# Optimization experiments

Hardware: AMD Instinct MI355X
Metric: run time of the kernel (lower is better)

The kernel has to match this reference:

```python
import jax, jax.numpy as jnp
import numpy as np

D = 512      # d_model
H = 8        # num_heads
HD = D // H  # head_dim = 64 (concat makes per-head dim 2*HD=128)
B = 32       # batch*group
T = 512      # time steps


def setup_inputs() -> dict:
    key = jax.random.key(0)
    ks = jax.random.split(key, 18)
    def W(k):
        return jax.random.normal(k, (D, D), dtype=jnp.float32) * 0.02
    inp = {
        "x_face": jax.random.normal(ks[0], (B, T, D), dtype=jnp.float32),
        "x_skeleton": jax.random.normal(ks[1], (B, T, D), dtype=jnp.float32),
        "wq1": W(ks[2]), "bq1": jnp.zeros((D,), jnp.float32),
        "wk1": W(ks[3]), "bk1": jnp.zeros((D,), jnp.float32),
        "wv1": W(ks[4]), "bv1": jnp.zeros((D,), jnp.float32),
        "wq2": W(ks[5]), "bq2": jnp.zeros((D,), jnp.float32),
        "wk2": W(ks[6]), "bk2": jnp.zeros((D,), jnp.float32),
        "wv2": W(ks[7]), "bv2": jnp.zeros((D,), jnp.float32),
        "wo1": W(ks[8]), "bo1": jnp.zeros((D,), jnp.float32),
        "wo2": W(ks[9]), "bo2": jnp.zeros((D,), jnp.float32),
    }
    return inp


def reference(x_face, x_skeleton,
              wq1, bq1, wk1, bk1, wv1, bv1,
              wq2, bq2, wk2, bk2, wv2, bv2,
              wo1, bo1, wo2, bo2):
    Bt, Tt, _ = x_face.shape

    def proj(x, w, b):
        # torch Linear: x @ W^T + b, then 'b t (h d) -> b h t d'
        return (x @ w.T + b).reshape(Bt, Tt, H, HD).transpose(0, 2, 1, 3)

    q = jnp.concatenate([proj(x_face, wq1, bq1), proj(x_skeleton, wq2, bq2)], axis=3)  # [B,H,T,2*HD]
    k = jnp.concatenate([proj(x_face, wk1, bk1), proj(x_skeleton, wk2, bk2)], axis=3)
    v = jnp.concatenate([proj(x_face, wv1, bv1), proj(x_skeleton, wv2, bv2)], axis=3)

    scores = jnp.einsum('bhid,bhjd->bhij', q, k) / (HD ** 0.5)  # scale by head_dim**0.5 as in source
    attn = jax.nn.softmax(scores, axis=-1)                      # dropout = identity (eval mode)
    out = jnp.einsum('bhij,bhjd->bhid', attn, v)                # [B,H,T,2*HD]
    out = out.transpose(0, 2, 1, 3).reshape(Bt, Tt, 2 * D)      # 'b h t d -> b t (h d)'

    x1, x2 = out[..., :D], out[..., D:]
    return (x1 @ wo1.T + bo1, x2 @ wo2.T + bo2)
```

## Files before the change

kernel.cpp:

```cpp
#include <hip/hip_runtime.h>
#include <hip/hip_bf16.h>
#include <stdint.h>

typedef __hip_bfloat16 bf16;
using f32x4 = __attribute__((ext_vector_type(4))) float;
using s16x8 = __attribute__((ext_vector_type(8))) short;

typedef __attribute__((address_space(1))) unsigned int gu32;
typedef __attribute__((address_space(3))) unsigned int lu32;

__device__ __forceinline__ void gll16(const void* g, void* l) {
  __builtin_amdgcn_global_load_lds((const gu32*)g, (lu32*)l, 16, 0, 0);
}

struct ConvJob { const float* src; bf16* dst; int n4; int pad; };
struct ConvParams { ConvJob j[10]; };
struct alignas(8) Bf4 { bf16 v[4]; };

__global__ void convert_kernel(ConvParams p) {
  ConvJob jb = p.j[blockIdx.z];
  int stride = gridDim.x * blockDim.x;
  for (int i = blockIdx.x * blockDim.x + threadIdx.x; i < jb.n4; i += stride) {
    float4 v = ((const float4*)jb.src)[i];
    Bf4 o;
    o.v[0] = __float2bfloat16(v.x);
    o.v[1] = __float2bfloat16(v.y);
    o.v[2] = __float2bfloat16(v.z);
    o.v[3] = __float2bfloat16(v.w);
    ((Bf4*)jb.dst)[i] = o;
  }
}

struct GemmSlice {
  const bf16* A; const bf16* W; const float* bias;
  bf16* dstQ; float* dstF;
  long lda; int dhalf; float scale; int mode;
};
struct GemmParams { GemmSlice s[6]; };

#define GSTAGE(kb) do { \
    _Pragma("unroll") \
    for (int i_ = 0; i_ < 4; ++i_) { \
      const int r0_ = w * 32 + i_ * 8; \
      gll16(Abase + (long)r0_ * lda + (kb) * 64, sA + r0_ * 64); \
      gll16(Wbase + (long)r0_ * 512 + (kb) * 64, sB + r0_ * 64); \
    } \
  } while (0)

#define GCOMPUTE() do { \
  _Pragma("unroll") \
  for (int ks = 0; ks < 2; ++ks) { \
    s16x8 af[4], bg[4]; \
    _Pragma("unroll") \
    for (int mi = 0; mi < 4; ++mi) { \
      const int row_ = wm + mi * 16 + fr; \
      af[mi] = *(const s16x8*)(sA + row_ * 64 + ((ks * 32 + fq * 8) ^ ((row_ & 7) << 3))); \
    } \
    _Pragma("unroll") \
    for (int ni = 0; ni < 4; ++ni) { \
      const int row_ = wn + ni * 16 + fr; \
      bg[ni] = *(const s16x8*)(sB + row_ * 64 + ((ks * 32 + fq * 8) ^ ((row_ & 7) << 3))); \
    } \
    __builtin_amdgcn_s_setprio(1); \
    _Pragma("unroll") \
    for (int mi = 0; mi < 4; ++mi) \
      _Pragma("unroll") \
      for (int ni = 0; ni < 4; ++ni) \
        acc[mi][ni] = __builtin_amdgcn_mfma_f32_16x16x32_bf16(af[mi], bg[ni], acc[mi][ni], 0, 0, 0); \
    __builtin_amdgcn_s_setprio(0); \
  } \
} while (0)

__global__ __launch_bounds__(256, 4) void gemm_kernel(GemmParams p) {
  __shared__ alignas(16) bf16 lds[16384];
  bf16* const sA = lds;
  bf16* const sB = lds + 8192;
  const GemmSlice sl = p.s[blockIdx.z];
  const long lda = sl.lda;
  const int tid = threadIdx.x;
  const int w = tid >> 6, ln = tid & 63;
  const int gm0 = blockIdx.x * 128;
  const int gn0 = blockIdx.y * 128;
  const int arow = ln >> 3;
  const int acolS = ((ln & 7) ^ (ln >> 3)) * 8;
  const int wm = (w >> 1) * 64, wn = (w & 1) * 64;
  const int fr = ln & 15, fq = ln >> 4;
  const bf16* const Abase = sl.A + (long)(gm0 + arow) * lda + acolS;
  const bf16* const Wbase = sl.W + (long)(gn0 + arow) * 512 + acolS;
  f32x4 acc[4][4] = {};

  for (int kb = 0; kb < 8; ++kb) {
    GSTAGE(kb);
    __syncthreads();
    GCOMPUTE();
    __syncthreads();
  }

  bf16* const eW = lds + w * 2304;
  if (sl.mode == 0) {
    const int col0 = gn0 + wn;
    const int h = col0 >> 6;
    const int bh = ((gm0 >> 9) << 3) + h;
    const int tb = (gm0 & 511) + wm;
#pragma unroll
    for (int ps = 0; ps < 2; ++ps) {
#pragma unroll
      for (int mi2 = 0; mi2 < 2; ++mi2) {
        const int mi = ps * 2 + mi2;
#pragma unroll
        for (int ni = 0; ni < 4; ++ni) {
          const float bia = sl.bias[col0 + ni * 16 + fr];
#pragma unroll
          for (int r = 0; r < 4; ++r)
            eW[(mi2 * 16 + fq * 4 + r) * 72 + ni * 16 + fr] =
                __float2bfloat16((acc[mi][ni][r] + bia) * sl.scale);
        }
      }
#pragma unroll
      for (int pp = 0; pp < 4; ++pp) {
        const int rr = pp * 8 + (ln >> 3);
        const s16x8 v = *(const s16x8*)(eW + rr * 72 + (ln & 7) * 8);
        *(s16x8*)(sl.dstQ + (((long)bh * 512 + tb + ps * 32 + rr) << 7) + sl.dhalf + (ln & 7) * 8) = v;
      }
    }
  } else if (sl.mode == 2) {
    const int col0 = gn0 + wn;
    const int h = col0 >> 6;
    const int bh = ((gm0 >> 9) << 3) + h;
    const int tb = (gm0 & 511) + wm;
#pragma unroll
    for (int ps = 0; ps < 2; ++ps) {
#pragma unroll
      for (int ni2 = 0; ni2 < 2; ++ni2) {
        const int ni = ps * 2 + ni2;
        const float bia = sl.bias[col0 + ni * 16 + fr];
#pragma unroll
        for (int mi = 0; mi < 4; ++mi) {
          Bf4 o;
#pragma unroll
          for (int r = 0; r < 4; ++r) o.v[r] = __float2bfloat16(acc[mi][ni][r] + bia);
          *(Bf4*)(eW + (ni2 * 16 + fr) * 72 + mi * 16 + fq * 4) = o;
        }
      }
#pragma unroll
      for (int pp = 0; pp < 4; ++pp) {
        const int rr = pp * 8 + (ln >> 3);
        const s16x8 v = *(const s16x8*)(eW + rr * 72 + (ln & 7) * 8);
        *(s16x8*)(sl.dstQ + (((long)bh * 128 + sl.dhalf + ps * 32 + rr) << 9) + tb + (ln & 7) * 8) = v;
      }
    }
  } else {
#pragma unroll
    for (int mi = 0; mi < 4; ++mi)
#pragma unroll
      for (int ni = 0; ni < 4; ++ni) {
        const int col = gn0 + wn + ni * 16 + fr;
        const float bia = sl.bias[col];
#pragma unroll
        for (int r = 0; r < 4; ++r) {
          const int row = gm0 + wm + mi * 16 + fq * 4 + r;
          sl.dstF[(long)row * 512 + col] = acc[mi][ni][r] + bia;
        }
      }
  }
}

#define STAGE(kt, bK, bV) do { \
    _Pragma("unroll") \
    for (int p_ = 0; p_ < 4; ++p_) \
      gll16(kgb + (kt) * 8192 + p_ * 2048, (bK) + tid * 8 + p_ * 2048); \
    _Pragma("unroll") \
    for (int p_ = 0; p_ < 4; ++p_) \
      gll16(vgb + (kt) * 64 + p_ * 16384, (bV) + tid * 8 + p_ * 2048); \
  } while (0)

#define COMPUTE(bK, bV) do { \
  f32x4 s2[2][4] = {}; \
  _Pragma("unroll") \
  for (int ks = 0; ks < 4; ++ks) { \
    _Pragma("unroll") \
    for (int ni = 0; ni < 4; ++ni) { \
      const int row_ = ni * 16 + fr; \
      const s16x8 kf = *(const s16x8*)((bK) + row_ * 128 + ((ks * 32 + fq * 8) ^ ((row_ & 7) << 3))); \
      _Pragma("unroll") \
      for (int mi = 0; mi < 2; ++mi) \
        s2[mi][ni] = __builtin_amdgcn_mfma_f32_16x16x32_bf16(qf[mi][ks], kf, s2[mi][ni], 0, 0, 0); \
    } \
  } \
  _Pragma("unroll") \
  for (int mi = 0; mi < 2; ++mi) \
    _Pragma("unroll") \
    for (int ni = 0; ni < 4; ++ni) \
      _Pragma("unroll") \
      for (int r = 0; r < 4; ++r) { \
        const int rp = mi * 16 + fq * 4 + r; \
        sPw[rp * 64 + ((ni * 16 + fr) ^ ((rp & 7) << 3))] = \
            __float2bfloat16(__builtin_amdgcn_exp2f(s2[mi][ni][r])); \
      } \
  _Pragma("unroll") \
  for (int ks = 0; ks < 2; ++ks) { \
    s16x8 pf[2]; \
    _Pragma("unroll") \
    for (int mi = 0; mi < 2; ++mi) { \
      const int row_ = mi * 16 + fr; \
      pf[mi] = *(const s16x8*)(sPw + row_ * 64 + ((ks * 32 + fq * 8) ^ ((row_ & 7) << 3))); \
      lracc[mi] = __builtin_amdgcn_mfma_f32_16x16x32_bf16(pf[mi], onesf, lracc[mi], 0, 0, 0); \
    } \
    _Pragma("unroll") \
    for (int nj = 0; nj < 8; ++nj) { \
      const int row_ = nj * 16 + fr; \
      const s16x8 vf = *(const s16x8*)((bV) + row_ * 64 + ((ks * 32 + fq * 8) ^ ((row_ & 7) << 3))); \
      _Pragma("unroll") \
      for (int mi = 0; mi < 2; ++mi) \
        o[mi][nj] = __builtin_amdgcn_mfma_f32_16x16x32_bf16(pf[mi], vf, o[mi][nj], 0, 0, 0); \
    } \
  } \
} while (0)

__global__ __launch_bounds__(256, 2) void attn_kernel(const bf16* __restrict__ Q,
                                                      const bf16* __restrict__ K,
                                                      const bf16* __restrict__ Vt,
                                                      bf16* __restrict__ AO) {
  __shared__ alignas(16) bf16 lds[40960];
  bf16* const ldsK0 = lds;
  bf16* const ldsV0 = lds + 8192;
  bf16* const ldsK1 = lds + 16384;
  bf16* const ldsV1 = lds + 24576;
  bf16* const sP    = lds + 32768;
  const int tid = threadIdx.x;
  const int w = tid >> 6, ln = tid & 63;
  const int fr = ln & 15, fq = ln >> 4;
  const int lg = (blockIdx.x & 7) * 128 + (blockIdx.x >> 3);
  const int bh = lg >> 2;
  const int q0 = (lg & 3) * 128;
  const long base = (long)bh << 16;
  bf16* const sPw = sP + w * 2048;

  const int kr0 = tid >> 4, kc = tid & 15;
  const int vr0 = tid >> 3, vc = tid & 7;
  const bf16* const kgb = K + base + kr0 * 128 + ((kc ^ (kr0 & 7)) * 8);
  const bf16* const vgb = Vt + base + (long)vr0 * 512 + ((vc ^ (vr0 & 7)) * 8);

  {
    const bf16* const qgb = Q + base + (long)q0 * 128 + kr0 * 128 + ((kc ^ (kr0 & 7)) * 8);
#pragma unroll
    for (int p = 0; p < 8; ++p)
      gll16(qgb + p * 2048, lds + tid * 8 + p * 2048);
  }
  __syncthreads();
  s16x8 qf[2][4];
#pragma unroll
  for (int mi = 0; mi < 2; ++mi) {
    const int row = w * 32 + mi * 16 + fr;
#pragma unroll
    for (int ks = 0; ks < 4; ++ks)
      qf[mi][ks] = *(const s16x8*)(lds + row * 128 + ((ks * 32 + fq * 8) ^ ((row & 7) << 3)));
  }
  __syncthreads();

  f32x4 o[2][8] = {};
  f32x4 lracc[2] = {};
  const short one_bf16 = (short)0x3F80;
  const s16x8 onesf = { one_bf16, one_bf16, one_bf16, one_bf16,
                        one_bf16, one_bf16, one_bf16, one_bf16 };

  STAGE(0, ldsK0, ldsV0);
  STAGE(1, ldsK1, ldsV1);

  for (int kt = 0; kt < 7; ++kt) {
    const bf16* bK = (kt & 1) ? ldsK1 : ldsK0;
    const bf16* bV = (kt & 1) ? ldsV1 : ldsV0;
    asm volatile("s_waitcnt vmcnt(8)" ::: "memory");
    __builtin_amdgcn_sched_barrier(0);
    __builtin_amdgcn_s_barrier();
    COMPUTE(bK, bV);
    asm volatile("s_waitcnt lgkmcnt(0)" ::: "memory");
    __builtin_amdgcn_sched_barrier(0);
    __builtin_amdgcn_s_barrier();
    if (kt < 6) STAGE(kt + 2, (bf16*)bK, (bf16*)bV);
  }
  asm volatile("s_waitcnt vmcnt(0)" ::: "memory");
  __builtin_amdgcn_sched_barrier(0);
  __builtin_amdgcn_s_barrier();
  COMPUTE(ldsK1, ldsV1);

  const int b = bh >> 3, h = bh & 7;
  float rl[2][4];
#pragma unroll
  for (int mi = 0; mi < 2; ++mi)
#pragma unroll
    for (int r = 0; r < 4; ++r) rl[mi][r] = 1.f / lracc[mi][r];
#pragma unroll
  for (int hh = 0; hh < 2; ++hh) {
#pragma unroll
    for (int mi = 0; mi < 2; ++mi)
#pragma unroll
      for (int nj4 = 0; nj4 < 4; ++nj4)
#pragma unroll
        for (int r = 0; r < 4; ++r) {
          const int rp = mi * 16 + fq * 4 + r;
          sPw[rp * 64 + ((nj4 * 16 + fr) ^ ((rp & 7) << 3))] =
              __float2bfloat16(o[mi][hh * 4 + nj4][r] * rl[mi][r]);
        }
#pragma unroll
    for (int pp = 0; pp < 4; ++pp) {
      const int rr = pp * 8 + (ln >> 3);
      const s16x8 v = *(const s16x8*)(sPw + rr * 64 + (((ln & 7) * 8) ^ ((rr & 7) << 3)));
      *(s16x8*)(AO + (((long)(b * 512 + q0 + w * 32 + rr)) << 10) + h * 128 + hh * 64 + (ln & 7) * 8) = v;
    }
  }
}

extern "C" void kernel_launch(void* const* d_in, const int* in_sizes, int n_in,
                              void* d_out, int out_size, void* d_ws, size_t ws_size,
                              hipStream_t stream) {
  const float* xf = (const float*)d_in[0];
  const float* xs = (const float*)d_in[1];
  const float* w_f[8] = { (const float*)d_in[2], (const float*)d_in[4], (const float*)d_in[6],
                          (const float*)d_in[8], (const float*)d_in[10], (const float*)d_in[12],
                          (const float*)d_in[14], (const float*)d_in[16] };

  bf16* ws = (bf16*)d_ws;
  bf16* XF = ws;
  bf16* XS = ws + 8388608;
  bf16* WW = ws + 16777216;
  bf16* Qb = ws + 18874368;
  bf16* Kb = Qb + 16777216;
  bf16* Vb = Kb + 16777216;
  bf16* AO = ws;

  ConvParams cp;
  cp.j[0] = { xf, XF, 2097152, 0 };
  cp.j[1] = { xs, XS, 2097152, 0 };
  for (int i = 0; i < 8; ++i) cp.j[2 + i] = { w_f[i], WW + i * 262144, 65536, 0 };
  convert_kernel<<<dim3(512, 1, 10), 256, 0, stream>>>(cp);

  const float qsc = 0.125f * 1.44269504088896f;
  GemmParams gp;
  gp.s[0] = { XF, WW + 0 * 262144, (const float*)d_in[3],  Qb, nullptr, 512, 0,  qsc, 0 };
  gp.s[1] = { XS, WW + 3 * 262144, (const float*)d_in[9],  Qb, nullptr, 512, 64, qsc, 0 };
  gp.s[2] = { XF, WW + 1 * 262144, (const float*)d_in[5],  Kb, nullptr, 512, 0,  1.f, 0 };
  gp.s[3] = { XS, WW + 4 * 262144, (const float*)d_in[11], Kb, nullptr, 512, 64, 1.f, 0 };
  gp.s[4] = { XF, WW + 2 * 262144, (const float*)d_in[7],  Vb, nullptr, 512, 0,  1.f, 2 };
  gp.s[5] = { XS, WW + 5 * 262144, (const float*)d_in[13], Vb, nullptr, 512, 64, 1.f, 2 };
  gemm_kernel<<<dim3(128, 4, 6), 256, 0, stream>>>(gp);

  attn_kernel<<<dim3(1024), 256, 0, stream>>>(Qb, Kb, Vb, AO);

  float* out = (float*)d_out;
  GemmParams op;
  op.s[0] = { AO,       WW + 6 * 262144, (const float*)d_in[15], nullptr, out,           1024, 0, 1.f, 1 };
  op.s[1] = { AO + 512, WW + 7 * 262144, (const float*)d_in[17], nullptr, out + 8388608, 1024, 0, 1.f, 1 };
  op.s[2] = op.s[0]; op.s[3] = op.s[0]; op.s[4] = op.s[0]; op.s[5] = op.s[0];
  gemm_kernel<<<dim3(128, 4, 2), 256, 0, stream>>>(op);
}
```

Before: 154.1 us.

## Replace LDS double buffer with register-staged prefetch in attention kernel

The attention kernel's K/V pipeline moves from two LDS buffers filled by direct global-to-LDS loads to one LDS buffer plus a register prefetch. The next tile is loaded into registers during compute and written to LDS after a barrier. This cuts LDS use per block from 80KB to 48KB, aiming at higher occupancy, but adds VGPR pressure, explicit LDS writes and an extra barrier per iteration. The wait counts must still cover the register loads correctly.

```diff
diff --git a/kernel.cpp b/kernel.cpp
--- a/kernel.cpp
+++ b/kernel.cpp
@@ -165,23 +165,37 @@
   }
 }
 
-#define STAGE(kt, bK, bV) do { \
+#define STAGE(kt) do { \
     _Pragma("unroll") \
     for (int p_ = 0; p_ < 4; ++p_) \
-      gll16(kgb + (kt) * 8192 + p_ * 2048, (bK) + tid * 8 + p_ * 2048); \
+      gll16(kgb + (kt) * 8192 + p_ * 2048, ldsK + tid * 8 + p_ * 2048); \
     _Pragma("unroll") \
     for (int p_ = 0; p_ < 4; ++p_) \
-      gll16(vgb + (kt) * 64 + p_ * 16384, (bV) + tid * 8 + p_ * 2048); \
+      gll16(vgb + (kt) * 64 + p_ * 16384, ldsV + tid * 8 + p_ * 2048); \
   } while (0)
 
-#define COMPUTE(bK, bV) do { \
+#define LOADR(kt) do { \
+    _Pragma("unroll") \
+    for (int p_ = 0; p_ < 4; ++p_) kreg[p_] = *(const s16x8*)(kgb + (kt) * 8192 + p_ * 2048); \
+    _Pragma("unroll") \
+    for (int p_ = 0; p_ < 4; ++p_) vreg[p_] = *(const s16x8*)(vgb + (kt) * 64 + p_ * 16384); \
+  } while (0)
+
+#define WRITER() do { \
+    _Pragma("unroll") \
+    for (int p_ = 0; p_ < 4; ++p_) *(s16x8*)(ldsK + tid * 8 + p_ * 2048) = kreg[p_]; \
+    _Pragma("unroll") \
+    for (int p_ = 0; p_ < 4; ++p_) *(s16x8*)(ldsV + tid * 8 + p_ * 2048) = vreg[p_]; \
+  } while (0)
+
+#define COMPUTE() do { \
   f32x4 s2[2][4] = {}; \
   _Pragma("unroll") \
   for (int ks = 0; ks < 4; ++ks) { \
     _Pragma("unroll") \
     for (int ni = 0; ni < 4; ++ni) { \
       const int row_ = ni * 16 + fr; \
-      const s16x8 kf = *(const s16x8*)((bK) + row_ * 128 + ((ks * 32 + fq * 8) ^ ((row_ & 7) << 3))); \
+      const s16x8 kf = *(const s16x8*)(ldsK + row_ * 128 + ((ks * 32 + fq * 8) ^ ((row_ & 7) << 3))); \
       _Pragma("unroll") \
       for (int mi = 0; mi < 2; ++mi) \
         s2[mi][ni] = __builtin_amdgcn_mfma_f32_16x16x32_bf16(qf[mi][ks], kf, s2[mi][ni], 0, 0, 0); \
@@ -209,7 +223,7 @@
     _Pragma("unroll") \
     for (int nj = 0; nj < 8; ++nj) { \
       const int row_ = nj * 16 + fr; \
-      const s16x8 vf = *(const s16x8*)((bV) + row_ * 64 + ((ks * 32 + fq * 8) ^ ((row_ & 7) << 3))); \
+      const s16x8 vf = *(const s16x8*)(ldsV + row_ * 64 + ((ks * 32 + fq * 8) ^ ((row_ & 7) << 3))); \
       _Pragma("unroll") \
       for (int mi = 0; mi < 2; ++mi) \
         o[mi][nj] = __builtin_amdgcn_mfma_f32_16x16x32_bf16(pf[mi], vf, o[mi][nj], 0, 0, 0); \
@@ -221,12 +235,10 @@
                                                       const bf16* __restrict__ K,
                                                       const bf16* __restrict__ Vt,
                                                       bf16* __restrict__ AO) {
-  __shared__ alignas(16) bf16 lds[40960];
-  bf16* const ldsK0 = lds;
-  bf16* const ldsV0 = lds + 8192;
-  bf16* const ldsK1 = lds + 16384;
-  bf16* const ldsV1 = lds + 24576;
-  bf16* const sP    = lds + 32768;
+  __shared__ alignas(16) bf16 lds[24576];
+  bf16* const ldsK = lds;
+  bf16* const ldsV = lds + 8192;
+  bf16* const sP   = lds + 16384;
   const int tid = threadIdx.x;
   const int w = tid >> 6, ln = tid & 63;
   const int fr = ln & 15, fq = ln >> 4;
@@ -263,26 +275,29 @@
   const short one_bf16 = (short)0x3F80;
   const s16x8 onesf = { one_bf16, one_bf16, one_bf16, one_bf16,
                         one_bf16, one_bf16, one_bf16, one_bf16 };
-
-  STAGE(0, ldsK0, ldsV0);
-  STAGE(1, ldsK1, ldsV1);
-
-  for (int kt = 0; kt < 7; ++kt) {
-    const bf16* bK = (kt & 1) ? ldsK1 : ldsK0;
-    const bf16* bV = (kt & 1) ? ldsV1 : ldsV0;
-    asm volatile("s_waitcnt vmcnt(8)" ::: "memory");
-    __builtin_amdgcn_sched_barrier(0);
-    __builtin_amdgcn_s_barrier();
-    COMPUTE(bK, bV);
+  s16x8 kreg[4], vreg[4];
+
+  STAGE(0);
+  __builtin_amdgcn_sched_barrier(0);
+  LOADR(1);
+  __builtin_amdgcn_sched_barrier(0);
+  asm volatile("s_waitcnt vmcnt(8)" ::: "memory");
+  __builtin_amdgcn_sched_barrier(0);
+  __builtin_amdgcn_s_barrier();
+
+  for (int kt = 0; kt < 8; ++kt) {
+    COMPUTE();
     asm volatile("s_waitcnt lgkmcnt(0)" ::: "memory");
     __builtin_amdgcn_sched_barrier(0);
     __builtin_amdgcn_s_barrier();
-    if (kt < 6) STAGE(kt + 2, (bf16*)bK, (bf16*)bV);
-  }
-  asm volatile("s_waitcnt vmcnt(0)" ::: "memory");
-  __builtin_amdgcn_sched_barrier(0);
-  __builtin_amdgcn_s_barrier();
-  COMPUTE(ldsK1, ldsV1);
+    if (kt < 7) {
+      WRITER();
+      if (kt < 6) LOADR(kt + 2);
+      asm volatile("s_waitcnt lgkmcnt(0)" ::: "memory");
+      __builtin_amdgcn_sched_barrier(0);
+      __builtin_amdgcn_s_barrier();
+    }
+  }
 
   const int b = bh >> 3, h = bh & 7;
   float rl[2][4];
```

Result: no change. 156.5 us (+1.6%).

## Double-buffer GEMM k-loop with async LDS loads and narrower K tiles

Applied to the files above, without the earlier changes.

Restructures the projection GEMM main loop from a single-buffered 64-wide K tile with two barriers per step into a double-buffered pipeline of 32-wide K tiles. Global-to-LDS loads for tile k+2 are issued while tile k is computed, gated by explicit vmcnt waits and barriers. The LDS swizzle is redone for the 32-column layout. This aims to hide global load latency behind MFMA work, at the cost of more iterations and barriers, each doing half the MFMA work.

```diff
diff --git a/kernel.cpp b/kernel.cpp
--- a/kernel.cpp
+++ b/kernel.cpp
@@ -38,62 +38,72 @@
 };
 struct GemmParams { GemmSlice s[6]; };
 
-#define GSTAGE(kb) do { \
-    _Pragma("unroll") \
-    for (int i_ = 0; i_ < 4; ++i_) { \
-      const int r0_ = w * 32 + i_ * 8; \
-      gll16(Abase + (long)r0_ * lda + (kb) * 64, sA + r0_ * 64); \
-      gll16(Wbase + (long)r0_ * 512 + (kb) * 64, sB + r0_ * 64); \
-    } \
+#define GSTAGE(kb, buf) do { \
+    const bf16* sa_ = Abase + (kb) * 32; \
+    const bf16* sb_ = Wbase + (kb) * 32; \
+    bf16* da_ = (buf) + tid * 8; \
+    bf16* db_ = (buf) + 4096 + tid * 8; \
+    gll16(sa_, da_); gll16(sa_ + (lda << 6), da_ + 2048); \
+    gll16(sb_, db_); gll16(sb_ + (512 << 6), db_ + 2048); \
   } while (0)
 
-#define GCOMPUTE() do { \
-  _Pragma("unroll") \
-  for (int ks = 0; ks < 2; ++ks) { \
-    s16x8 af[4], bg[4]; \
-    _Pragma("unroll") \
-    for (int mi = 0; mi < 4; ++mi) { \
-      const int row_ = wm + mi * 16 + fr; \
-      af[mi] = *(const s16x8*)(sA + row_ * 64 + ((ks * 32 + fq * 8) ^ ((row_ & 7) << 3))); \
-    } \
-    _Pragma("unroll") \
-    for (int ni = 0; ni < 4; ++ni) { \
-      const int row_ = wn + ni * 16 + fr; \
-      bg[ni] = *(const s16x8*)(sB + row_ * 64 + ((ks * 32 + fq * 8) ^ ((row_ & 7) << 3))); \
-    } \
-    __builtin_amdgcn_s_setprio(1); \
-    _Pragma("unroll") \
-    for (int mi = 0; mi < 4; ++mi) \
-      _Pragma("unroll") \
-      for (int ni = 0; ni < 4; ++ni) \
-        acc[mi][ni] = __builtin_amdgcn_mfma_f32_16x16x32_bf16(af[mi], bg[ni], acc[mi][ni], 0, 0, 0); \
-    __builtin_amdgcn_s_setprio(0); \
-  } \
+#define GCOMPUTE(bA, bB) do { \
+  s16x8 af[4], bg[4]; \
+  _Pragma("unroll") \
+  for (int mi = 0; mi < 4; ++mi) \
+    af[mi] = *(const s16x8*)((bA) + (wm + mi * 16 + fr) * 32 + cw); \
+  _Pragma("unroll") \
+  for (int ni = 0; ni < 4; ++ni) \
+    bg[ni] = *(const s16x8*)((bB) + (wn + ni * 16 + fr) * 32 + cw); \
+  __builtin_amdgcn_s_setprio(1); \
+  _Pragma("unroll") \
+  for (int mi = 0; mi < 4; ++mi) \
+    _Pragma("unroll") \
+    for (int ni = 0; ni < 4; ++ni) \
+      acc[mi][ni] = __builtin_amdgcn_mfma_f32_16x16x32_bf16(af[mi], bg[ni], acc[mi][ni], 0, 0, 0); \
+  __builtin_amdgcn_s_setprio(0); \
 } while (0)
 
 __global__ __launch_bounds__(256, 4) void gemm_kernel(GemmParams p) {
   __shared__ alignas(16) bf16 lds[16384];
-  bf16* const sA = lds;
-  bf16* const sB = lds + 8192;
   const GemmSlice sl = p.s[blockIdx.z];
   const long lda = sl.lda;
   const int tid = threadIdx.x;
   const int w = tid >> 6, ln = tid & 63;
   const int gm0 = blockIdx.x * 128;
   const int gn0 = blockIdx.y * 128;
-  const int arow = ln >> 3;
-  const int acolS = ((ln & 7) ^ (ln >> 3)) * 8;
   const int wm = (w >> 1) * 64, wn = (w & 1) * 64;
   const int fr = ln & 15, fq = ln >> 4;
-  const bf16* const Abase = sl.A + (long)(gm0 + arow) * lda + acolS;
-  const bf16* const Wbase = sl.W + (long)(gn0 + arow) * 512 + acolS;
+  const int r0 = tid >> 2;
+  const int c0 = ((tid & 3) ^ ((r0 >> 1) & 3)) * 8;
+  const bf16* const Abase = sl.A + (long)(gm0 + r0) * lda + c0;
+  const bf16* const Wbase = sl.W + (long)(gn0 + r0) * 512 + c0;
+  const int cw = (fq ^ ((fr >> 1) & 3)) * 8;
   f32x4 acc[4][4] = {};
 
-  for (int kb = 0; kb < 8; ++kb) {
-    GSTAGE(kb);
-    __syncthreads();
-    GCOMPUTE();
-    __syncthreads();
+  GSTAGE(0, lds);
+  GSTAGE(1, lds + 8192);
+  asm volatile("s_waitcnt vmcnt(4)" ::: "memory");
+  __builtin_amdgcn_sched_barrier(0);
+  __builtin_amdgcn_s_barrier();
+
+#pragma unroll
+  for (int kt = 0; kt < 16; ++kt) {
+    bf16* const buf = lds + ((kt & 1) ? 8192 : 0);
+    GCOMPUTE(buf, buf + 4096);
+    asm volatile("s_waitcnt lgkmcnt(0)" ::: "memory");
+    __builtin_amdgcn_sched_barrier(0);
+    __builtin_amdgcn_s_barrier();
+    if (kt < 14) {
+      GSTAGE(kt + 2, buf);
+      asm volatile("s_waitcnt vmcnt(4)" ::: "memory");
+      __builtin_amdgcn_sched_barrier(0);
+      __builtin_amdgcn_s_barrier();
+    } else if (kt == 14) {
+      asm volatile("s_waitcnt vmcnt(0)" ::: "memory");
+      __builtin_amdgcn_sched_barrier(0);
+      __builtin_amdgcn_s_barrier();
+    }
   }
 
   bf16* const eW = lds + w * 2304;
```

After: 161.3 us. 4.7% more time.
